# Performance work log

Hardware: AMD Instinct MI355X
Metric: run time of the kernel (lower is better)

Reference implementation:

```python
import jax, jax.numpy as jnp
import numpy as np

NUM_DOCS = 1024  # fill_max of doc_indices

def setup_inputs() -> dict:
    key = jax.random.key(0)
    k1, k2, k3 = jax.random.split(key, 3)
    N, D, E = 262144, 1024, 64
    x = jax.random.normal(k1, (N, D), dtype=jnp.float32)
    doc_indices = jax.random.randint(k2, (N,), 0, NUM_DOCS, dtype=jnp.int64)
    W_gate = jax.random.normal(k3, (E, D), dtype=jnp.float32)
    return {"x": x, "doc_indices": doc_indices, "W_gate": W_gate}

def reference(x, doc_indices, W_gate):
    # gate linear + softmax: [N, E]
    logits = jnp.einsum('nd,ed->ne', x, W_gate)
    w = jax.nn.softmax(logits, axis=-1)

    seg = doc_indices.astype(jnp.int32)
    E = w.shape[-1]
    # one-pass segment reductions replacing the per-document Python loop
    sum_w = jax.ops.segment_sum(w, seg, num_segments=NUM_DOCS)          # [D, E]
    sum_w2 = jax.ops.segment_sum(w * w, seg, num_segments=NUM_DOCS)     # [D, E]
    counts = jax.ops.segment_sum(jnp.ones_like(w[:, :1]), seg, num_segments=NUM_DOCS)  # [D, 1]
    safe_n = jnp.maximum(counts, 1.0)
    centroid = sum_w / safe_n                                            # [D, E]
    # per-doc sum of squared deviations: sum(w^2) - n * centroid^2
    ssd = jnp.sum(sum_w2 - safe_n * centroid * centroid, axis=-1)        # [D]
    n = counts[:, 0]
    per_doc_mse = ssd / (safe_n[:, 0] * E)                               # mean over n_d*E elements
    valid = n > 1.0                                                      # docs with >1 token contribute
    penalty_sum = jnp.sum(jnp.where(valid, per_doc_mse, 0.0))
    num_unique = jnp.sum((n > 0.0).astype(jnp.float32))
    doc_penalty = penalty_sum / num_unique
    return (w, doc_penalty)
```

## Files before the change

kernel.cpp:

```cpp
#include <hip/hip_runtime.h>
#include <math.h>

#define NROWS 262144
#define DDIM  1024
#define EEXP  64
#define NDOCS 1024
#define BM    128
#define BK    32
#define HB    64
#define RPB   (NROWS / HB)

typedef __attribute__((ext_vector_type(8)))  __bf16 bf16x8;
typedef __attribute__((ext_vector_type(16))) float  f32x16;
typedef unsigned short ushort_t;
typedef unsigned int   uint_t;


__global__ __launch_bounds__(1024) void init_kernel(int* cnt, float* pen_sum, float* uniq) {
    const int t = threadIdx.x;
    cnt[t] = 0;
    if (t == 0) { pen_sum[0] = 0.0f; uniq[0] = 0.0f; }
}

__global__ __launch_bounds__(256) void hist_kernel(const int* __restrict__ idx, int* __restrict__ cnt) {
    __shared__ int lh[NDOCS];
    const int t = threadIdx.x;
    for (int i = t; i < NDOCS; i += 256) lh[i] = 0;
    __syncthreads();
    const int base = blockIdx.x * RPB;
    for (int i = t; i < RPB; i += 256) atomicAdd(&lh[idx[base + i]], 1);
    __syncthreads();
    for (int i = t; i < NDOCS; i += 256) {
        const int c = lh[i];
        if (c) atomicAdd(&cnt[i], c);
    }
}

__global__ __launch_bounds__(1024) void scan_kernel(const int* __restrict__ cnt,
                                                    int* __restrict__ offsets,
                                                    int* __restrict__ cursor) {
    __shared__ int sbuf[NDOCS];
    const int t = threadIdx.x;
    const int my = cnt[t];
    sbuf[t] = my;
    __syncthreads();
    for (int off = 1; off < NDOCS; off <<= 1) {
        int add = (t >= off) ? sbuf[t - off] : 0;
        __syncthreads();
        sbuf[t] += add;
        __syncthreads();
    }
    const int excl = sbuf[t] - my;
    offsets[t] = excl;
    cursor[t]  = excl;
    if (t == NDOCS - 1) offsets[NDOCS] = sbuf[t];
}

__global__ __launch_bounds__(256) void scatter_kernel(const int* __restrict__ idx,
                                                      int* __restrict__ cursor,
                                                      int* __restrict__ sorted_rows) {
    __shared__ int lh[NDOCS];
    __shared__ int lbase[NDOCS];
    __shared__ int lc[NDOCS];
    const int t = threadIdx.x;
    for (int i = t; i < NDOCS; i += 256) { lh[i] = 0; lc[i] = 0; }
    __syncthreads();
    const int base = blockIdx.x * RPB;
    for (int i = t; i < RPB; i += 256) atomicAdd(&lh[idx[base + i]], 1);
    __syncthreads();
    for (int i = t; i < NDOCS; i += 256) {
        const int c = lh[i];
        if (c) lbase[i] = atomicAdd(&cursor[i], c);
    }
    __syncthreads();
    for (int i = t; i < RPB; i += 256) {
        const int r = base + i;
        const int d = idx[r];
        const int p = atomicAdd(&lc[d], 1);
        sorted_rows[lbase[d] + p] = r;
    }
}

__global__ __launch_bounds__(256) void convw_frag_kernel(const float* __restrict__ Wg,
                                                         ushort_t* __restrict__ Wf) {
    const int idx = blockIdx.x * 256 + threadIdx.x;
    const int j = idx & 7;
    const int l = (idx >> 3) & 63;
    const int f = (idx >> 9) & 7;
    const int T = idx >> 12;
    const int cl = l & 31;
    const int hi = l >> 5;
    const int e  = cl + 32 * ((f >> 1) & 1);
    const int k  = T * 32 + 16 * (f & 1) + 8 * hi + j;
    const float wv = Wg[e * DDIM + k];
    const uint_t b = __float_as_uint(wv);
    ushort_t out;
    if (f < 4) {
        out = (ushort_t)(b >> 16);
    } else {
        const float lov = wv - __uint_as_float(b & 0xFFFF0000u);
        out = (ushort_t)(__float_as_uint(lov) >> 16);
    }
    Wf[idx] = out;
}

__device__ __forceinline__ void gl2lds16(const float* g, float* l) {
    __builtin_amdgcn_global_load_lds(
        (const __attribute__((address_space(1))) void*)g,
        (__attribute__((address_space(3))) void*)l,
        16, 0, 0);
}

#define VMCNT(N)  asm volatile("s_waitcnt vmcnt(" #N ")" ::: "memory")

struct WT { bf16x8 h00, h01, h10, h11, m00, m01, m10, m11; };

__global__ __launch_bounds__(256, 2) void gemm_softmax_kernel(
    const float*    __restrict__ x,
    const ushort_t* __restrict__ Wf,
    float*          __restrict__ w_out)
{
    __shared__ float xs[3][4096];

    const int t   = threadIdx.x;
    const int w   = t >> 6;
    const int l   = t & 63;
    const int cl  = l & 31;
    const int hi  = l >> 5;
    const size_t br = (size_t)blockIdx.x * BM;

    const int lrow  = l >> 3;
    const int lunit = l & 7;

    f32x16 acc0 = {};
    f32x16 acc1 = {};
    WT wA, wB;

    union u8b { uint_t u[4]; bf16x8 v; };

#define LOAD_WF(DST, T2) do {                                                          \
        const ushort_t* p_ = Wf + ((size_t)(T2) * 8 * 64 + l) * 8;                     \
        DST.h00 = *(const bf16x8*)(p_ + 0 * 512);                                      \
        DST.h01 = *(const bf16x8*)(p_ + 1 * 512);                                      \
        DST.h10 = *(const bf16x8*)(p_ + 2 * 512);                                      \
        DST.h11 = *(const bf16x8*)(p_ + 3 * 512);                                      \
        DST.m00 = *(const bf16x8*)(p_ + 4 * 512);                                      \
        DST.m01 = *(const bf16x8*)(p_ + 5 * 512);                                      \
        DST.m10 = *(const bf16x8*)(p_ + 6 * 512);                                      \
        DST.m11 = *(const bf16x8*)(p_ + 7 * 512);                                      \
    } while (0)

#define STAGE_X(BUF, k0) do {                                                          \
        float* xb_ = &xs[BUF][w * 1024];                                               \
        _Pragma("unroll")                                                              \
        for (int i_ = 0; i_ < 4; ++i_) {                                               \
            const int row_ = i_ * 8 + lrow;                                            \
            const float* gp_ = x + (br + w * 32 + row_) * DDIM + (k0) + ((lunit ^ lrow) * 4); \
            gl2lds16(gp_, xb_ + i_ * 256);                                             \
        } } while (0)

#define SPLIT8(A, B, AH, AL) do {                                                      \
        const float av_[8] = {A.x, A.y, A.z, A.w, B.x, B.y, B.z, B.w};                 \
        _Pragma("unroll")                                                              \
        for (int p_ = 0; p_ < 4; ++p_) {                                               \
            const uint_t b0_ = __float_as_uint(av_[2 * p_]);                           \
            const uint_t b1_ = __float_as_uint(av_[2 * p_ + 1]);                       \
            AH.u[p_] = (b0_ >> 16) | (b1_ & 0xFFFF0000u);                              \
            const float l0_ = av_[2 * p_]     - __uint_as_float(b0_ & 0xFFFF0000u);    \
            const float l1_ = av_[2 * p_ + 1] - __uint_as_float(b1_ & 0xFFFF0000u);    \
            AL.u[p_] = (__float_as_uint(l0_) >> 16) | (__float_as_uint(l1_) & 0xFFFF0000u); \
        } } while (0)

#define COMPUTE(BUF, WV) do {                                                          \
        const float* xb_ = &xs[BUF][w * 1024];                                         \
        const int sw7_ = cl & 7;                                                       \
        const float4 a0_ = *(const float4*)&xb_[cl * 32 + (((2*hi + 0) ^ sw7_) * 4)];  \
        const float4 a1_ = *(const float4*)&xb_[cl * 32 + (((2*hi + 1) ^ sw7_) * 4)];  \
        const float4 a2_ = *(const float4*)&xb_[cl * 32 + (((4 + 2*hi + 0) ^ sw7_) * 4)]; \
        const float4 a3_ = *(const float4*)&xb_[cl * 32 + (((4 + 2*hi + 1) ^ sw7_) * 4)]; \
        u8b ah0, al0, ah1, al1;                                                        \
        SPLIT8(a0_, a1_, ah0, al0);                                                    \
        SPLIT8(a2_, a3_, ah1, al1);                                                    \
        acc0 = __builtin_amdgcn_mfma_f32_32x32x16_bf16(ah0.v, WV.h00, acc0, 0, 0, 0);  \
        acc1 = __builtin_amdgcn_mfma_f32_32x32x16_bf16(ah0.v, WV.h10, acc1, 0, 0, 0);  \
        acc0 = __builtin_amdgcn_mfma_f32_32x32x16_bf16(ah0.v, WV.m00, acc0, 0, 0, 0);  \
        acc1 = __builtin_amdgcn_mfma_f32_32x32x16_bf16(ah0.v, WV.m10, acc1, 0, 0, 0);  \
        acc0 = __builtin_amdgcn_mfma_f32_32x32x16_bf16(al0.v, WV.h00, acc0, 0, 0, 0);  \
        acc1 = __builtin_amdgcn_mfma_f32_32x32x16_bf16(al0.v, WV.h10, acc1, 0, 0, 0);  \
        acc0 = __builtin_amdgcn_mfma_f32_32x32x16_bf16(ah1.v, WV.h01, acc0, 0, 0, 0);  \
        acc1 = __builtin_amdgcn_mfma_f32_32x32x16_bf16(ah1.v, WV.h11, acc1, 0, 0, 0);  \
        acc0 = __builtin_amdgcn_mfma_f32_32x32x16_bf16(ah1.v, WV.m01, acc0, 0, 0, 0);  \
        acc1 = __builtin_amdgcn_mfma_f32_32x32x16_bf16(ah1.v, WV.m11, acc1, 0, 0, 0);  \
        acc0 = __builtin_amdgcn_mfma_f32_32x32x16_bf16(al1.v, WV.h01, acc0, 0, 0, 0);  \
        acc1 = __builtin_amdgcn_mfma_f32_32x32x16_bf16(al1.v, WV.h11, acc1, 0, 0, 0);  \
    } while (0)

    LOAD_WF(wA, 0);
    STAGE_X(0, 0);
    STAGE_X(1, BK);

    LOAD_WF(wB, 1);
    STAGE_X(2, 2 * BK);
    VMCNT(16);
    COMPUTE(0, wA);

    int rb = 1;
    #pragma unroll 1
    for (int tp = 0; tp < 14; ++tp) {
        const int t1 = 2 * tp + 1;
        {
            const int wb1 = (rb + 2) % 3;
            LOAD_WF(wA, t1 + 1);
            STAGE_X(wb1, (t1 + 2) * BK);
            VMCNT(24);
            COMPUTE(rb, wB);
        }
        const int rb2 = (rb == 2) ? 0 : rb + 1;
        {
            const int wb2 = (rb2 + 2) % 3;
            LOAD_WF(wB, t1 + 2);
            STAGE_X(wb2, (t1 + 3) * BK);
            VMCNT(24);
            COMPUTE(rb2, wA);
        }
        rb = (rb2 == 2) ? 0 : rb2 + 1;
    }
    LOAD_WF(wA, 30);
    STAGE_X(1, 31 * BK);
    VMCNT(24);
    COMPUTE(2, wB);
    LOAD_WF(wB, 31);
    VMCNT(20);
    COMPUTE(0, wA);
    VMCNT(8);
    COMPUTE(1, wB);

    const size_t orow_base = br + (size_t)w * 32;
    #pragma unroll
    for (int r = 0; r < 16; ++r) {
        const int row = (r & 3) + 8 * (r >> 2) + 4 * hi;
        const float v0 = acc0[r];
        const float v1 = acc1[r];
        float m = fmaxf(v0, v1);
        m = fmaxf(m, __shfl_xor(m, 1));
        m = fmaxf(m, __shfl_xor(m, 2));
        m = fmaxf(m, __shfl_xor(m, 4));
        m = fmaxf(m, __shfl_xor(m, 8));
        m = fmaxf(m, __shfl_xor(m, 16));
        const float e0 = __expf(v0 - m);
        const float e1 = __expf(v1 - m);
        float s = e0 + e1;
        s += __shfl_xor(s, 1);
        s += __shfl_xor(s, 2);
        s += __shfl_xor(s, 4);
        s += __shfl_xor(s, 8);
        s += __shfl_xor(s, 16);
        const float inv = 1.0f / s;
        float* wo = w_out + (orow_base + row) * EEXP;
        wo[cl]      = e0 * inv;
        wo[32 + cl] = e1 * inv;
    }
#undef LOAD_WF
#undef STAGE_X
#undef SPLIT8
#undef COMPUTE
}

__global__ __launch_bounds__(256) void segsum_kernel(
    const float* __restrict__ w,
    const int*   __restrict__ sorted_rows,
    const int*   __restrict__ offsets,
    float*       __restrict__ pen_sum,
    float*       __restrict__ uniq)
{
    __shared__ int rows_s[512];
    __shared__ float ls1[4][64], ls2[4][64];

    const int d  = blockIdx.x;
    const int t  = threadIdx.x;
    const int e  = t & 63;
    const int rg = t >> 6;
    const int start = offsets[d];
    const int end   = offsets[d + 1];
    const int n     = end - start;

    for (int i = t; i < n && i < 512; i += 256) rows_s[i] = sorted_rows[start + i];
    __syncthreads();

    float s1 = 0.0f, s2 = 0.0f;
    for (int i = rg; i < n; i += 4) {
        const int row = (i < 512) ? rows_s[i] : sorted_rows[start + i];
        const float v = w[(size_t)row * EEXP + e];
        s1 += v;
        s2 += v * v;
    }

    ls1[rg][e] = s1;
    ls2[rg][e] = s2;
    __syncthreads();

    if (t < 64) {
        const float a = ls1[0][e] + ls1[1][e] + ls1[2][e] + ls1[3][e];
        const float b = ls2[0][e] + ls2[1][e] + ls2[2][e] + ls2[3][e];
        const float safe = fmaxf((float)n, 1.0f);
        float contrib = b - a * a / safe;
        #pragma unroll
        for (int off = 32; off > 0; off >>= 1)
            contrib += __shfl_down(contrib, off);
        if (e == 0) {
            if (n > 1) atomicAdd(pen_sum, contrib / (safe * (float)EEXP));
            if (n > 0) atomicAdd(uniq, 1.0f);
        }
    }
}

__global__ void final_kernel(const float* __restrict__ pen_sum,
                             const float* __restrict__ uniq,
                             float* __restrict__ pen_out) {
    pen_out[0] = pen_sum[0] / uniq[0];
}

extern "C" void kernel_launch(void* const* d_in, const int* in_sizes, int n_in,
                              void* d_out, int out_size, void* d_ws, size_t ws_size,
                              hipStream_t stream) {
    const float* x   = (const float*)d_in[0];
    const int*   idx = (const int*)d_in[1];
    const float* Wg  = (const float*)d_in[2];

    float* out   = (float*)d_out;
    float* w_out = out;
    float* pen   = out + (size_t)NROWS * EEXP;

    ushort_t* Wf = (ushort_t*)d_ws;
    int* sorted_rows = (int*)(Wf + 131072);
    int* offsets     = sorted_rows + NROWS;
    int* cnt         = offsets + NDOCS + 1;
    int* cursor      = cnt + NDOCS;
    float* pen_sum   = (float*)(cursor + NDOCS);
    float* uniq      = pen_sum + 1;

    init_kernel<<<1, 1024, 0, stream>>>(cnt, pen_sum, uniq);
    hist_kernel<<<HB, 256, 0, stream>>>(idx, cnt);
    scan_kernel<<<1, 1024, 0, stream>>>(cnt, offsets, cursor);
    scatter_kernel<<<HB, 256, 0, stream>>>(idx, cursor, sorted_rows);
    convw_frag_kernel<<<131072 / 256, 256, 0, stream>>>(Wg, Wf);
    gemm_softmax_kernel<<<NROWS / BM, 256, 0, stream>>>(x, Wf, w_out);
    segsum_kernel<<<NDOCS, 256, 0, stream>>>(w_out, sorted_rows, offsets, pen_sum, uniq);
    final_kernel<<<1, 1, 0, stream>>>(pen_sum, uniq, pen);
}
```

Before: 367.8 us.

## Fuse preprocessing kernels, merge scatter into GEMM grid, finalize via last-block

Result: no change. 370.0 us (+0.6%).

```diff
diff --git a/kernel.cpp b/kernel.cpp
--- a/kernel.cpp
+++ b/kernel.cpp
@@ -9,6 +9,7 @@
 #define BK    32
 #define HB    64
 #define RPB   (NROWS / HB)
+#define NGEMM (NROWS / BM)
 
 typedef __attribute__((ext_vector_type(8)))  __bf16 bf16x8;
 typedef __attribute__((ext_vector_type(16))) float  f32x16;
@@ -16,32 +17,54 @@
 typedef unsigned int   uint_t;
 
 
-__global__ __launch_bounds__(1024) void init_kernel(int* cnt, float* pen_sum, float* uniq) {
-    const int t = threadIdx.x;
-    cnt[t] = 0;
-    if (t == 0) { pen_sum[0] = 0.0f; uniq[0] = 0.0f; }
-}
-
-__global__ __launch_bounds__(256) void hist_kernel(const int* __restrict__ idx, int* __restrict__ cnt) {
-    __shared__ int lh[NDOCS];
-    const int t = threadIdx.x;
-    for (int i = t; i < NDOCS; i += 256) lh[i] = 0;
-    __syncthreads();
-    const int base = blockIdx.x * RPB;
-    for (int i = t; i < RPB; i += 256) atomicAdd(&lh[idx[base + i]], 1);
-    __syncthreads();
-    for (int i = t; i < NDOCS; i += 256) {
-        const int c = lh[i];
-        if (c) atomicAdd(&cnt[i], c);
-    }
-}
-
-__global__ __launch_bounds__(1024) void scan_kernel(const int* __restrict__ cnt,
+__global__ __launch_bounds__(256) void conv_hist_kernel(const float* __restrict__ Wg,
+                                                        ushort_t* __restrict__ Wf,
+                                                        const int* __restrict__ idx,
+                                                        int* __restrict__ hist_slices) {
+    if (blockIdx.x < 512) {
+        const int i = blockIdx.x * 256 + threadIdx.x;
+        const int j = i & 7;
+        const int l = (i >> 3) & 63;
+        const int f = (i >> 9) & 7;
+        const int T = i >> 12;
+        const int cl = l & 31;
+        const int hi = l >> 5;
+        const int e  = cl + 32 * ((f >> 1) & 1);
+        const int k  = T * 32 + 16 * (f & 1) + 8 * hi + j;
+        const float wv = Wg[e * DDIM + k];
+        const uint_t b = __float_as_uint(wv);
+        ushort_t out;
+        if (f < 4) {
+            out = (ushort_t)(b >> 16);
+        } else {
+            const float lov = wv - __uint_as_float(b & 0xFFFF0000u);
+            out = (ushort_t)(__float_as_uint(lov) >> 16);
+        }
+        Wf[i] = out;
+    } else {
+        __shared__ int lh[NDOCS];
+        const int bh = blockIdx.x - 512;
+        const int t  = threadIdx.x;
+        for (int i = t; i < NDOCS; i += 256) lh[i] = 0;
+        __syncthreads();
+        const int base = bh * RPB;
+        for (int i = t; i < RPB; i += 256) atomicAdd(&lh[idx[base + i]], 1);
+        __syncthreads();
+        for (int i = t; i < NDOCS; i += 256) hist_slices[bh * NDOCS + i] = lh[i];
+    }
+}
+
+__global__ __launch_bounds__(1024) void scan_kernel(const int* __restrict__ hist_slices,
                                                     int* __restrict__ offsets,
-                                                    int* __restrict__ cursor) {
+                                                    int* __restrict__ cursor,
+                                                    float* __restrict__ pen_sum,
+                                                    float* __restrict__ uniq,
+                                                    int* __restrict__ done_count) {
     __shared__ int sbuf[NDOCS];
     const int t = threadIdx.x;
-    const int my = cnt[t];
+    int my = 0;
+    #pragma unroll 4
+    for (int b = 0; b < HB; ++b) my += hist_slices[b * NDOCS + t];
     sbuf[t] = my;
     __syncthreads();
     for (int off = 1; off < NDOCS; off <<= 1) {
@@ -54,54 +77,7 @@
     offsets[t] = excl;
     cursor[t]  = excl;
     if (t == NDOCS - 1) offsets[NDOCS] = sbuf[t];
-}
-
-__global__ __launch_bounds__(256) void scatter_kernel(const int* __restrict__ idx,
-                                                      int* __restrict__ cursor,
-                                                      int* __restrict__ sorted_rows) {
-    __shared__ int lh[NDOCS];
-    __shared__ int lbase[NDOCS];
-    __shared__ int lc[NDOCS];
-    const int t = threadIdx.x;
-    for (int i = t; i < NDOCS; i += 256) { lh[i] = 0; lc[i] = 0; }
-    __syncthreads();
-    const int base = blockIdx.x * RPB;
-    for (int i = t; i < RPB; i += 256) atomicAdd(&lh[idx[base + i]], 1);
-    __syncthreads();
-    for (int i = t; i < NDOCS; i += 256) {
-        const int c = lh[i];
-        if (c) lbase[i] = atomicAdd(&cursor[i], c);
-    }
-    __syncthreads();
-    for (int i = t; i < RPB; i += 256) {
-        const int r = base + i;
-        const int d = idx[r];
-        const int p = atomicAdd(&lc[d], 1);
-        sorted_rows[lbase[d] + p] = r;
-    }
-}
-
-__global__ __launch_bounds__(256) void convw_frag_kernel(const float* __restrict__ Wg,
-                                                         ushort_t* __restrict__ Wf) {
-    const int idx = blockIdx.x * 256 + threadIdx.x;
-    const int j = idx & 7;
-    const int l = (idx >> 3) & 63;
-    const int f = (idx >> 9) & 7;
-    const int T = idx >> 12;
-    const int cl = l & 31;
-    const int hi = l >> 5;
-    const int e  = cl + 32 * ((f >> 1) & 1);
-    const int k  = T * 32 + 16 * (f & 1) + 8 * hi + j;
-    const float wv = Wg[e * DDIM + k];
-    const uint_t b = __float_as_uint(wv);
-    ushort_t out;
-    if (f < 4) {
-        out = (ushort_t)(b >> 16);
-    } else {
-        const float lov = wv - __uint_as_float(b & 0xFFFF0000u);
-        out = (ushort_t)(__float_as_uint(lov) >> 16);
-    }
-    Wf[idx] = out;
+    if (t == 0) { pen_sum[0] = 0.0f; uniq[0] = 0.0f; done_count[0] = 0; }
 }
 
 __device__ __forceinline__ void gl2lds16(const float* g, float* l) {
@@ -115,12 +91,40 @@
 
 struct WT { bf16x8 h00, h01, h10, h11, m00, m01, m10, m11; };
 
-__global__ __launch_bounds__(256, 2) void gemm_softmax_kernel(
+__global__ __launch_bounds__(256, 3) void gemm_scatter_kernel(
     const float*    __restrict__ x,
     const ushort_t* __restrict__ Wf,
+    const int*      __restrict__ idx,
+    int*            __restrict__ cursor,
+    int*            __restrict__ sorted_rows,
     float*          __restrict__ w_out)
 {
     __shared__ float xs[3][4096];
+
+    if (blockIdx.x >= NGEMM) {
+        int* lh    = (int*)&xs[0][0];
+        int* lbase = lh + NDOCS;
+        int* lc    = lbase + NDOCS;
+        const int bh = blockIdx.x - NGEMM;
+        const int t  = threadIdx.x;
+        for (int i = t; i < NDOCS; i += 256) { lh[i] = 0; lc[i] = 0; }
+        __syncthreads();
+        const int base = bh * RPB;
+        for (int i = t; i < RPB; i += 256) atomicAdd(&lh[idx[base + i]], 1);
+        __syncthreads();
+        for (int i = t; i < NDOCS; i += 256) {
+            const int c = lh[i];
+            if (c) lbase[i] = atomicAdd(&cursor[i], c);
+        }
+        __syncthreads();
+        for (int i = t; i < RPB; i += 256) {
+            const int r = base + i;
+            const int d = idx[r];
+            const int p = atomicAdd(&lc[d], 1);
+            sorted_rows[lbase[d] + p] = r;
+        }
+        return;
+    }
 
     const int t   = threadIdx.x;
     const int w   = t >> 6;
@@ -266,12 +270,14 @@
 #undef COMPUTE
 }
 
-__global__ __launch_bounds__(256) void segsum_kernel(
+__global__ __launch_bounds__(256) void segsum_final_kernel(
     const float* __restrict__ w,
     const int*   __restrict__ sorted_rows,
     const int*   __restrict__ offsets,
     float*       __restrict__ pen_sum,
-    float*       __restrict__ uniq)
+    float*       __restrict__ uniq,
+    int*         __restrict__ done_count,
+    float*       __restrict__ pen_out)
 {
     __shared__ int rows_s[512];
     __shared__ float ls1[4][64], ls2[4][64];
@@ -312,12 +318,15 @@
             if (n > 0) atomicAdd(uniq, 1.0f);
         }
     }
-}
-
-__global__ void final_kernel(const float* __restrict__ pen_sum,
-                             const float* __restrict__ uniq,
-                             float* __restrict__ pen_out) {
-    pen_out[0] = pen_sum[0] / uniq[0];
+    __syncthreads();
+    if (t == 0) {
+        __threadfence();
+        const int prev = atomicAdd(done_count, 1);
+        if (prev == NDOCS - 1) {
+            __threadfence();
+            pen_out[0] = pen_sum[0] / uniq[0];
+        }
+    }
 }
 
 extern "C" void kernel_launch(void* const* d_in, const int* in_sizes, int n_in,
@@ -331,20 +340,17 @@
     float* w_out = out;
     float* pen   = out + (size_t)NROWS * EEXP;
 
-    ushort_t* Wf = (ushort_t*)d_ws;
-    int* sorted_rows = (int*)(Wf + 131072);
+    ushort_t* Wf     = (ushort_t*)d_ws;
+    int* hist_slices = (int*)(Wf + 131072);
+    int* sorted_rows = hist_slices + HB * NDOCS;
     int* offsets     = sorted_rows + NROWS;
-    int* cnt         = offsets + NDOCS + 1;
-    int* cursor      = cnt + NDOCS;
+    int* cursor      = offsets + NDOCS + 1;
     float* pen_sum   = (float*)(cursor + NDOCS);
     float* uniq      = pen_sum + 1;
-
-    init_kernel<<<1, 1024, 0, stream>>>(cnt, pen_sum, uniq);
-    hist_kernel<<<HB, 256, 0, stream>>>(idx, cnt);
-    scan_kernel<<<1, 1024, 0, stream>>>(cnt, offsets, cursor);
-    scatter_kernel<<<HB, 256, 0, stream>>>(idx, cursor, sorted_rows);
-    convw_frag_kernel<<<131072 / 256, 256, 0, stream>>>(Wg, Wf);
-    gemm_softmax_kernel<<<NROWS / BM, 256, 0, stream>>>(x, Wf, w_out);
-    segsum_kernel<<<NDOCS, 256, 0, stream>>>(w_out, sorted_rows, offsets, pen_sum, uniq);
-    final_kernel<<<1, 1, 0, stream>>>(pen_sum, uniq, pen);
-}
+    int* done_count  = (int*)(uniq + 1);
+
+    conv_hist_kernel<<<512 + HB, 256, 0, stream>>>(Wg, Wf, idx, hist_slices);
+    scan_kernel<<<1, 1024, 0, stream>>>(hist_slices, offsets, cursor, pen_sum, uniq, done_count);
+    gemm_scatter_kernel<<<NGEMM + HB, 256, 0, stream>>>(x, Wf, idx, cursor, sorted_rows, w_out);
+    segsum_final_kernel<<<NDOCS, 256, 0, stream>>>(w_out, sorted_rows, offsets, pen_sum, uniq, done_count, pen);
+}
```
